# Kernel optimization log

Measured on AMD Instinct MI355X. Metric: run time of the kernel, lower is better.

The kernel has to match this reference:

```python
import jax, jax.numpy as jnp
import numpy as np

BETA = 0.9
TH = 1.0  # snn.Leaky default threshold
SPARSITY = 0.5


@jax.custom_vjp
def spike(x):
    # Heaviside spike; surrogate (atan, alpha=2) gradient as in snntorch default
    return (x > 0).astype(x.dtype)

def _spike_fwd(x):
    return spike(x), x

def _spike_bwd(x, g):
    return (g / (1.0 + (jnp.pi * x) ** 2),)

spike.defvjp(_spike_fwd, _spike_bwd)


def setup_inputs() -> dict:
    key = jax.random.key(0)
    ks = jax.random.split(key, 6)
    T, B, NIN, NH, NOUT = 50, 512, 784, 1000, 10

    def mk_w(k, o, i):
        k1, k2 = jax.random.split(k)
        w = jax.random.normal(k1, (o, i), jnp.float32) * (1.0 / np.sqrt(i))
        mask = (jax.random.uniform(k2, (o, i)) > SPARSITY).astype(jnp.float32)
        return w * mask

    x = jax.random.normal(ks[0], (T, B, NIN), jnp.float32)
    return dict(
        x=x,
        W0=mk_w(ks[1], NH, NIN), b0=jnp.zeros((NH,), jnp.float32),
        W1=mk_w(ks[2], NH, NH), b1=jnp.zeros((NH,), jnp.float32),
        W2=mk_w(ks[3], NH, NH), b2=jnp.zeros((NH,), jnp.float32),
        W3=mk_w(ks[4], NOUT, NH), b3=jnp.zeros((NOUT,), jnp.float32),
    )


def reference(x, W0, b0, W1, b1, W2, b2, W3, b3):
    params = ((W0, b0), (W1, b1), (W2, b2), (W3, b3))
    B = x.shape[1]
    mems0 = tuple(jnp.zeros((B, W.shape[0]), x.dtype) for W, _ in params)

    def step(mems, xt):
        inp = xt
        new_mems, spks = [], []
        for (W, b), m in zip(params, mems):
            cur = inp @ W.T + b
            # snntorch Leaky (reset_mechanism='subtract'):
            # reset from previous mem (detached), then mem = beta*mem + I - reset*th
            reset = jax.lax.stop_gradient((m > TH).astype(x.dtype))
            m_new = BETA * m + cur - reset * TH
            s = spike(m_new - TH)
            new_mems.append(m_new)
            spks.append(s)
            inp = s
        return tuple(new_mems), (tuple(spks), tuple(new_mems))

    _, (spk_rec, mem_rec) = jax.lax.scan(step, mems0, x)
    # spk_rec/mem_rec: tuples of [T, B, dim] arrays per layer
    return (*spk_rec, *mem_rec)
```

## Files before the change

kernel.cpp:

```cpp
#include <hip/hip_runtime.h>


typedef int int4v  __attribute__((ext_vector_type(4)));
typedef int int16v __attribute__((ext_vector_type(16)));

#define XSCALE 68719476736.0
#define WSCALE 1099511627776.0
#define MT 25600

__global__ void wsplit_i8(const float* __restrict__ W, signed char* __restrict__ out,
                          int Nreal, int Npad, int K, int Kpad)
{
    int idx = blockIdx.x * blockDim.x + threadIdx.x;
    int total = Npad * Kpad;
    if (idx >= total) return;
    int n = idx / Kpad, k = idx - n * Kpad;
    long long v = 0;
    if (n < Nreal && k < K) v = __double2ll_rn((double)W[(size_t)n * K + k] * WSCALE);
    size_t plane = (size_t)total;
#pragma unroll
    for (int p = 0; p < 4; ++p) {
        int d = (int)(v & 255); if (d > 127) d -= 256;
        out[p * plane + idx] = (signed char)d;
        v = (v - d) >> 8;
    }
    out[4 * plane + idx] = (signed char)v;
}

__global__ void xsplit_all(const float* __restrict__ x, signed char* __restrict__ out)
{
    int idx = blockIdx.x * blockDim.x + threadIdx.x;
    if (idx >= MT * 832) return;
    int row = idx / 832, k = idx - row * 832;
    long long v = 0;
    if (k < 784) v = __double2ll_rn((double)x[(size_t)row * 784 + k] * XSCALE);
    const size_t plane = (size_t)MT * 832;
    signed char* o = out + idx;
#pragma unroll
    for (int p = 0; p < 4; ++p) {
        int d = (int)(v & 255); if (d > 127) d -= 256;
        o[p * plane] = (signed char)d;
        v = (v - d) >> 8;
    }
    o[4 * plane] = (signed char)v;
}

template<int NA, int KP, int CS>
__global__ __launch_bounds__(256)
void gemm32(const signed char* __restrict__ Ap, size_t planeA,
            const signed char* __restrict__ Wp, size_t planeW,
            double* __restrict__ curout)
{
    __shared__ __align__(16) signed char Wld[5 * 64 * 80];
    __shared__ __align__(16) signed char Ald[NA * 64 * 80];
    constexpr int NIT = KP / 64;

    const int tid = threadIdx.x;
    const int l   = tid & 63;
    const int w   = tid >> 6;
    const int wm  = (w & 1) * 32;
    const int wn  = (w >> 1) * 32;
    const int r32 = l & 31;
    const int h   = l >> 5;

    const int bm = blockIdx.y * 64;
    const int bn = blockIdx.x * 64;

    const int srow = tid >> 2;
    const int sc   = (tid & 3) * 16;

    const signed char* ag = Ap + (size_t)(bm + srow) * KP + sc;
    const signed char* wg = Wp + (size_t)(bn + srow) * KP + sc;

    int4v Ar[NA], Wr[5];
#pragma unroll
    for (int p = 0; p < 5; ++p)  Wr[p] = *(const int4v*)(wg + p * planeW);
#pragma unroll
    for (int p = 0; p < NA; ++p) Ar[p] = *(const int4v*)(ag + p * planeA);

    int16v acc[5];
#pragma unroll
    for (int s = 0; s < 5; ++s)
#pragma unroll
        for (int r = 0; r < 16; ++r) acc[s][r] = 0;

    for (int it = 0; it < NIT; ++it) {
        __syncthreads();
#pragma unroll
        for (int p = 0; p < 5; ++p)
            *(int4v*)&Wld[(p * 64 + srow) * 80 + sc] = Wr[p];
#pragma unroll
        for (int p = 0; p < NA; ++p)
            *(int4v*)&Ald[(p * 64 + srow) * 80 + sc] = Ar[p];
        __syncthreads();

        if (it + 1 < NIT) {
            int kb = (it + 1) * 64;
#pragma unroll
            for (int p = 0; p < 5; ++p)
                Wr[p] = *(const int4v*)(wg + kb + p * planeW);
#pragma unroll
            for (int p = 0; p < NA; ++p)
                Ar[p] = *(const int4v*)(ag + kb + p * planeA);
        }

#pragma unroll
        for (int k2 = 0; k2 < 2; ++k2) {
            const int off = k2 * 32 + 16 * h;
            if constexpr (NA == 5) {
                int4v af[5], bq[5];
#pragma unroll
                for (int p = 0; p < 5; ++p)
                    af[p] = *(const int4v*)&Ald[(p * 64 + wm + r32) * 80 + off];
#pragma unroll
                for (int q = 0; q < 5; ++q)
                    bq[q] = *(const int4v*)&Wld[(q * 64 + wn + r32) * 80 + off];
#pragma unroll
                for (int q = 0; q < 5; ++q)
#pragma unroll
                    for (int p = 0; p < 5; ++p)
                        if (p + q >= 4)
                            acc[p + q - 4] = __builtin_amdgcn_mfma_i32_32x32x32_i8(
                                af[p], bq[q], acc[p + q - 4], 0, 0, 0);
            } else {
                int4v a0 = *(const int4v*)&Ald[(wm + r32) * 80 + off];
#pragma unroll
                for (int q = 0; q < 5; ++q) {
                    int4v bq = *(const int4v*)&Wld[(q * 64 + wn + r32) * 80 + off];
                    acc[q] = __builtin_amdgcn_mfma_i32_32x32x32_i8(a0, bq, acc[q], 0, 0, 0);
                }
            }
        }
    }

    const int col = bn + wn + r32;
    if (col < CS) {
#pragma unroll
        for (int reg = 0; reg < 16; ++reg) {
            int row = bm + wm + (reg & 3) + 8 * (reg >> 2) + 4 * h;
            double v = (double)acc[4][reg];
            v = v * 256.0 + (double)acc[3][reg];
            v = v * 256.0 + (double)acc[2][reg];
            v = v * 256.0 + (double)acc[1][reg];
            v = v * 256.0 + (double)acc[0][reg];
            curout[(size_t)row * CS + col] = v * (NA == 5 ? 0x1p-44 : 0x1p-40);
        }
    }
}

template<int KP>
__global__ __launch_bounds__(256)
void gemm32w(const signed char* __restrict__ Asp,
             const signed char* __restrict__ Wp, size_t planeW,
             double* __restrict__ curout)
{
    __shared__ __align__(16) signed char Wld[2][5 * 64 * 80];
    __shared__ __align__(16) signed char Ald[2][128 * 80];
    constexpr int NIT = KP / 64;

    const int tid = threadIdx.x;
    const int l   = tid & 63;
    const int w   = tid >> 6;
    const int wm  = (w & 1) * 64;
    const int wn  = (w >> 1) * 32;
    const int r32 = l & 31;
    const int h   = l >> 5;

    const int bm = blockIdx.y * 128;
    const int bn = blockIdx.x * 64;

    const int srA = tid >> 1;
    const int scA = (tid & 1) * 32;
    const int srW = tid >> 2;
    const int scW = (tid & 3) * 16;

    const signed char* ag = Asp + (size_t)(bm + srA) * KP + scA;
    const signed char* wg = Wp  + (size_t)(bn + srW) * KP + scW;

    int4v Ar0 = *(const int4v*)(ag);
    int4v Ar1 = *(const int4v*)(ag + 16);
    int4v Wr[5];
#pragma unroll
    for (int p = 0; p < 5; ++p) Wr[p] = *(const int4v*)(wg + p * planeW);
#pragma unroll
    for (int p = 0; p < 5; ++p)
        *(int4v*)&Wld[0][(p * 64 + srW) * 80 + scW] = Wr[p];
    *(int4v*)&Ald[0][srA * 80 + scA]      = Ar0;
    *(int4v*)&Ald[0][srA * 80 + scA + 16] = Ar1;
    if (NIT > 1) {
        Ar0 = *(const int4v*)(ag + 64);
        Ar1 = *(const int4v*)(ag + 64 + 16);
#pragma unroll
        for (int p = 0; p < 5; ++p)
            Wr[p] = *(const int4v*)(wg + 64 + p * planeW);
    }
    __syncthreads();

    int16v acc[2][5];
#pragma unroll
    for (int mi = 0; mi < 2; ++mi)
#pragma unroll
        for (int s = 0; s < 5; ++s)
#pragma unroll
            for (int r = 0; r < 16; ++r) acc[mi][s][r] = 0;

    for (int it = 0; it < NIT; ++it) {
        const int cur = it & 1;

#pragma unroll
        for (int k2 = 0; k2 < 2; ++k2) {
            const int off = k2 * 32 + 16 * h;
            int4v bq[5];
#pragma unroll
            for (int q = 0; q < 5; ++q)
                bq[q] = *(const int4v*)&Wld[cur][(q * 64 + wn + r32) * 80 + off];
#pragma unroll
            for (int mi = 0; mi < 2; ++mi) {
                int4v a0 = *(const int4v*)&Ald[cur][(wm + mi * 32 + r32) * 80 + off];
#pragma unroll
                for (int q = 0; q < 5; ++q)
                    acc[mi][q] = __builtin_amdgcn_mfma_i32_32x32x32_i8(
                        a0, bq[q], acc[mi][q], 0, 0, 0);
            }
        }

        if (it + 1 < NIT) {
            const int nxt = cur ^ 1;
#pragma unroll
            for (int p = 0; p < 5; ++p)
                *(int4v*)&Wld[nxt][(p * 64 + srW) * 80 + scW] = Wr[p];
            *(int4v*)&Ald[nxt][srA * 80 + scA]      = Ar0;
            *(int4v*)&Ald[nxt][srA * 80 + scA + 16] = Ar1;
            if (it + 2 < NIT) {
                int kb = (it + 2) * 64;
                Ar0 = *(const int4v*)(ag + kb);
                Ar1 = *(const int4v*)(ag + kb + 16);
#pragma unroll
                for (int p = 0; p < 5; ++p)
                    Wr[p] = *(const int4v*)(wg + kb + p * planeW);
            }
            __syncthreads();
        }
    }

    const int col = bn + wn + r32;
#pragma unroll
    for (int mi = 0; mi < 2; ++mi)
#pragma unroll
        for (int reg = 0; reg < 16; ++reg) {
            int row = bm + wm + mi * 32 + (reg & 3) + 8 * (reg >> 2) + 4 * h;
            double v = (double)acc[mi][4][reg];
            v = v * 256.0 + (double)acc[mi][3][reg];
            v = v * 256.0 + (double)acc[mi][2][reg];
            v = v * 256.0 + (double)acc[mi][1][reg];
            v = v * 256.0 + (double)acc[mi][0][reg];
            curout[(size_t)row * 1024 + col] = v * 0x1p-40;
        }
}

__global__ __launch_bounds__(256)
void if_update(const double* __restrict__ cur, const float* __restrict__ bias,
               float* __restrict__ spk, float* __restrict__ mem,
               signed char* __restrict__ spk_i8)
{
    int idx = blockIdx.x * blockDim.x + threadIdx.x;
    if (idx >= 512 * 512) return;
    int row = idx >> 9, col = (idx & 511) * 2;
    if (col >= 1000) {
        for (int t = 0; t < 50; ++t)
            *(short*)&spk_i8[((size_t)t * 512 + row) * 1024 + col] = 0;
        return;
    }
    double mp0 = 0.0, mp1 = 0.0;
    double bs0 = (double)bias[col], bs1 = (double)bias[col + 1];
    for (int t = 0; t < 50; ++t) {
        double2 c = *(const double2*)&cur[((size_t)t * 512 + row) * 1024 + col];
        double rst0 = (mp0 > 1.0) ? 1.0 : 0.0;
        double rst1 = (mp1 > 1.0) ? 1.0 : 0.0;
        double mn0 = 0.9 * mp0 + (c.x + bs0) - rst0;
        double mn1 = 0.9 * mp1 + (c.y + bs1) - rst1;
        int s0 = (mn0 > 1.0) ? 1 : 0;
        int s1 = (mn1 > 1.0) ? 1 : 0;
        size_t o = ((size_t)t * 512 + row) * 1000 + col;
        *(float2*)&spk[o] = make_float2((float)s0, (float)s1);
        *(float2*)&mem[o] = make_float2((float)mn0, (float)mn1);
        *(short*)&spk_i8[((size_t)t * 512 + row) * 1024 + col] =
            (short)(s0 | (s1 << 8));
        mp0 = mn0; mp1 = mn1;
    }
}

__global__ __launch_bounds__(256)
void if3_kernel(const double* __restrict__ cur3, const float* __restrict__ bias,
                float* __restrict__ spk3, float* __restrict__ mem3)
{
    int idx = blockIdx.x * blockDim.x + threadIdx.x;
    if (idx >= 5120) return;
    int brow = idx / 10, col = idx - brow * 10;
    double bs = (double)bias[col];
    double mp = 0.0;
    for (int t = 0; t < 50; ++t) {
        double c   = cur3[((size_t)t * 512 + brow) * 16 + col] + bs;
        double rst = (mp > 1.0) ? 1.0 : 0.0;
        double mn  = 0.9 * mp + c - rst;
        size_t o   = (size_t)t * 5120 + (size_t)brow * 10 + col;
        spk3[o] = (mn > 1.0) ? 1.0f : 0.0f;
        mem3[o] = (float)mn;
        mp = mn;
    }
}

extern "C" void kernel_launch(void* const* d_in, const int* in_sizes, int n_in,
                              void* d_out, int out_size, void* d_ws, size_t ws_size,
                              hipStream_t stream)
{
    const float* x  = (const float*)d_in[0];
    const float* W0 = (const float*)d_in[1];
    const float* b0 = (const float*)d_in[2];
    const float* W1 = (const float*)d_in[3];
    const float* b1 = (const float*)d_in[4];
    const float* W2 = (const float*)d_in[5];
    const float* b2 = (const float*)d_in[6];
    const float* W3 = (const float*)d_in[7];
    const float* b3 = (const float*)d_in[8];
    float* out = (float*)d_out;

    const int T = 50;
    const size_t LNH = (size_t)512 * 1000;
    const size_t LNO = (size_t)512 * 10;

    float* spk0 = out;
    float* spk1 = spk0 + (size_t)T * LNH;
    float* spk2 = spk1 + (size_t)T * LNH;
    float* spk3 = spk2 + (size_t)T * LNH;
    float* mem0 = spk3 + (size_t)T * LNO;
    float* mem1 = mem0 + (size_t)T * LNH;
    float* mem2 = mem1 + (size_t)T * LNH;
    float* mem3 = mem2 + (size_t)T * LNH;

    double* cur = (double*)d_ws;
    signed char* W0d = (signed char*)(cur + (size_t)MT * 1024);
    signed char* W1d = W0d + (size_t)5 * 1024 * 832;
    signed char* W2d = W1d + (size_t)5 * 1024 * 1024;
    signed char* W3d = W2d + (size_t)5 * 1024 * 1024;
    signed char* xsb = W3d + (size_t)5 * 64 * 1024;
    signed char* sp0 = xsb + (size_t)5 * MT * 832;
    signed char* sp1 = sp0 + (size_t)MT * 1024;
    signed char* sp2 = sp1 + (size_t)MT * 1024;

    wsplit_i8<<<(1024 * 832  + 255) / 256, 256, 0, stream>>>(W0, W0d, 1000, 1024, 784,  832);
    wsplit_i8<<<(1024 * 1024 + 255) / 256, 256, 0, stream>>>(W1, W1d, 1000, 1024, 1000, 1024);
    wsplit_i8<<<(1024 * 1024 + 255) / 256, 256, 0, stream>>>(W2, W2d, 1000, 1024, 1000, 1024);
    wsplit_i8<<<(64 * 1024   + 255) / 256, 256, 0, stream>>>(W3, W3d, 10,   64,   1000, 1024);

    xsplit_all<<<(MT * 832 + 255) / 256, 256, 0, stream>>>(x, xsb);

    const size_t plA0 = (size_t)MT * 832;
    const size_t plW0 = (size_t)1024 * 832;
    const size_t plWH = (size_t)1024 * 1024;
    const size_t plW3 = (size_t)64 * 1024;

    dim3 blk(256);
    dim3 g0(16, MT / 64);
    dim3 gW(16, MT / 128);
    dim3 g3(1, MT / 64);

    gemm32<5, 832, 1024><<<g0, blk, 0, stream>>>(xsb, plA0, W0d, plW0, cur);
    if_update<<<1024, 256, 0, stream>>>(cur, b0, spk0, mem0, sp0);
    gemm32w<1024><<<gW, blk, 0, stream>>>(sp0, W1d, plWH, cur);
    if_update<<<1024, 256, 0, stream>>>(cur, b1, spk1, mem1, sp1);
    gemm32w<1024><<<gW, blk, 0, stream>>>(sp1, W2d, plWH, cur);
    if_update<<<1024, 256, 0, stream>>>(cur, b2, spk2, mem2, sp2);
    gemm32<1, 1024, 16><<<g3, blk, 0, stream>>>(sp2, 0, W3d, plW3, cur);
    if3_kernel<<<20, 256, 0, stream>>>(cur, b3, spk3, mem3);
}
```

Measured before the change: 1.061 ms.

## Pre-tile hidden-layer operands and stream them into LDS with direct global loads

```diff
diff --git a/kernel.cpp b/kernel.cpp
--- a/kernel.cpp
+++ b/kernel.cpp
@@ -7,6 +7,13 @@
 #define XSCALE 68719476736.0
 #define WSCALE 1099511627776.0
 #define MT 25600
+
+__device__ __forceinline__ void gload16(const signed char* g, signed char* l)
+{
+    __builtin_amdgcn_global_load_lds(
+        (const __attribute__((address_space(1))) void*)g,
+        (__attribute__((address_space(3))) void*)l, 16, 0, 0);
+}
 
 __global__ void wsplit_i8(const float* __restrict__ W, signed char* __restrict__ out,
                           int Nreal, int Npad, int K, int Kpad)
@@ -25,6 +32,34 @@
         v = (v - d) >> 8;
     }
     out[4 * plane + idx] = (signed char)v;
+}
+
+__global__ void wsplit_tw(const float* __restrict__ W, signed char* __restrict__ out)
+{
+    int idx = blockIdx.x * blockDim.x + threadIdx.x;
+    if (idx >= 65536) return;
+    int q4 = idx & 3, row = (idx >> 2) & 63, kb = (idx >> 8) & 15, nt = idx >> 12;
+    int n = nt * 64 + row;
+    long long v[16];
+#pragma unroll
+    for (int j = 0; j < 16; ++j) {
+        int k = kb * 64 + q4 * 16 + j;
+        float wv = (n < 1000 && k < 1000) ? W[(size_t)n * 1000 + k] : 0.f;
+        v[j] = __double2ll_rn((double)wv * WSCALE);
+    }
+    signed char* tile = out + (size_t)(nt * 16 + kb) * 25600;
+#pragma unroll
+    for (int p = 0; p < 5; ++p) {
+        signed char pk[16];
+#pragma unroll
+        for (int j = 0; j < 16; ++j) {
+            int d;
+            if (p < 4) { d = (int)(v[j] & 255); if (d > 127) d -= 256; v[j] = (v[j] - d) >> 8; }
+            else d = (int)v[j];
+            pk[j] = (signed char)d;
+        }
+        *(int4v*)&tile[(p * 64 + row) * 80 + q4 * 16] = *(const int4v*)pk;
+    }
 }
 
 __global__ void xsplit_all(const float* __restrict__ x, signed char* __restrict__ out)
@@ -148,15 +183,14 @@
     }
 }
 
-template<int KP>
 __global__ __launch_bounds__(256)
-void gemm32w(const signed char* __restrict__ Asp,
-             const signed char* __restrict__ Wp, size_t planeW,
-             double* __restrict__ curout)
-{
-    __shared__ __align__(16) signed char Wld[2][5 * 64 * 80];
-    __shared__ __align__(16) signed char Ald[2][128 * 80];
-    constexpr int NIT = KP / 64;
+void gemm32wa(const signed char* __restrict__ At,
+              const signed char* __restrict__ Wt,
+              double* __restrict__ curout)
+{
+    constexpr int NIT = 16;
+    __shared__ __align__(16) signed char B0[36864];
+    __shared__ __align__(16) signed char B1[36864];
 
     const int tid = threadIdx.x;
     const int l   = tid & 63;
@@ -166,35 +200,24 @@
     const int r32 = l & 31;
     const int h   = l >> 5;
 
-    const int bm = blockIdx.y * 128;
-    const int bn = blockIdx.x * 64;
-
-    const int srA = tid >> 1;
-    const int scA = (tid & 1) * 32;
-    const int srW = tid >> 2;
-    const int scW = (tid & 3) * 16;
-
-    const signed char* ag = Asp + (size_t)(bm + srA) * KP + scA;
-    const signed char* wg = Wp  + (size_t)(bn + srW) * KP + scW;
-
-    int4v Ar0 = *(const int4v*)(ag);
-    int4v Ar1 = *(const int4v*)(ag + 16);
-    int4v Wr[5];
-#pragma unroll
-    for (int p = 0; p < 5; ++p) Wr[p] = *(const int4v*)(wg + p * planeW);
-#pragma unroll
-    for (int p = 0; p < 5; ++p)
-        *(int4v*)&Wld[0][(p * 64 + srW) * 80 + scW] = Wr[p];
-    *(int4v*)&Ald[0][srA * 80 + scA]      = Ar0;
-    *(int4v*)&Ald[0][srA * 80 + scA + 16] = Ar1;
-    if (NIT > 1) {
-        Ar0 = *(const int4v*)(ag + 64);
-        Ar1 = *(const int4v*)(ag + 64 + 16);
-#pragma unroll
-        for (int p = 0; p < 5; ++p)
-            Wr[p] = *(const int4v*)(wg + 64 + p * planeW);
-    }
-    __syncthreads();
+    const int nt = blockIdx.x, mt = blockIdx.y;
+    const signed char* wtile = Wt + (size_t)nt * (16 * 25600);
+    const signed char* atile = At + (size_t)mt * (16 * 10240);
+
+    auto issue = [&](int kb, signed char* buf) {
+        const signed char* wsrc = wtile + kb * 25600;
+        const signed char* asrc = atile + kb * 10240;
+#pragma unroll
+        for (int j = 0; j < 9; ++j) {
+            int c = w + 4 * j;
+            const signed char* g;
+            signed char* d;
+            if (c < 25) { g = wsrc + c * 1024;                     d = buf + c * 1024; }
+            else        { int ac = c - 25;
+                          g = asrc + (ac < 10 ? ac : 9) * 1024;    d = buf + 25600 + ac * 1024; }
+            gload16(g + l * 16, d);
+        }
+    };
 
     int16v acc[2][5];
 #pragma unroll
@@ -204,51 +227,47 @@
 #pragma unroll
             for (int r = 0; r < 16; ++r) acc[mi][s][r] = 0;
 
+    issue(0, B0);
+    issue(1, B1);
+    asm volatile("s_waitcnt vmcnt(9)" ::: "memory");
+    __builtin_amdgcn_s_barrier();
+
     for (int it = 0; it < NIT; ++it) {
-        const int cur = it & 1;
-
+        signed char* buf = (it & 1) ? B1 : B0;
 #pragma unroll
         for (int k2 = 0; k2 < 2; ++k2) {
             const int off = k2 * 32 + 16 * h;
             int4v bq[5];
 #pragma unroll
             for (int q = 0; q < 5; ++q)
-                bq[q] = *(const int4v*)&Wld[cur][(q * 64 + wn + r32) * 80 + off];
+                bq[q] = *(const int4v*)&buf[(q * 64 + wn + r32) * 80 + off];
 #pragma unroll
             for (int mi = 0; mi < 2; ++mi) {
-                int4v a0 = *(const int4v*)&Ald[cur][(wm + mi * 32 + r32) * 80 + off];
+                int4v a0 = *(const int4v*)&buf[25600 + (wm + mi * 32 + r32) * 80 + off];
 #pragma unroll
                 for (int q = 0; q < 5; ++q)
                     acc[mi][q] = __builtin_amdgcn_mfma_i32_32x32x32_i8(
                         a0, bq[q], acc[mi][q], 0, 0, 0);
             }
         }
-
         if (it + 1 < NIT) {
-            const int nxt = cur ^ 1;
-#pragma unroll
-            for (int p = 0; p < 5; ++p)
-                *(int4v*)&Wld[nxt][(p * 64 + srW) * 80 + scW] = Wr[p];
-            *(int4v*)&Ald[nxt][srA * 80 + scA]      = Ar0;
-            *(int4v*)&Ald[nxt][srA * 80 + scA + 16] = Ar1;
+            __builtin_amdgcn_s_barrier();
             if (it + 2 < NIT) {
-                int kb = (it + 2) * 64;
-                Ar0 = *(const int4v*)(ag + kb);
-                Ar1 = *(const int4v*)(ag + kb + 16);
-#pragma unroll
-                for (int p = 0; p < 5; ++p)
-                    Wr[p] = *(const int4v*)(wg + kb + p * planeW);
+                issue(it + 2, buf);
+                asm volatile("s_waitcnt vmcnt(9)" ::: "memory");
+            } else {
+                asm volatile("s_waitcnt vmcnt(0)" ::: "memory");
             }
-            __syncthreads();
-        }
-    }
-
-    const int col = bn + wn + r32;
+            __builtin_amdgcn_s_barrier();
+        }
+    }
+
+    const int col = nt * 64 + wn + r32;
 #pragma unroll
     for (int mi = 0; mi < 2; ++mi)
 #pragma unroll
         for (int reg = 0; reg < 16; ++reg) {
-            int row = bm + wm + mi * 32 + (reg & 3) + 8 * (reg >> 2) + 4 * h;
+            int row = mt * 128 + wm + mi * 32 + (reg & 3) + 8 * (reg >> 2) + 4 * h;
             double v = (double)acc[mi][4][reg];
             v = v * 256.0 + (double)acc[mi][3][reg];
             v = v * 256.0 + (double)acc[mi][2][reg];
@@ -258,6 +277,7 @@
         }
 }
 
+template<bool TILED>
 __global__ __launch_bounds__(256)
 void if_update(const double* __restrict__ cur, const float* __restrict__ bias,
                float* __restrict__ spk, float* __restrict__ mem,
@@ -266,9 +286,19 @@
     int idx = blockIdx.x * blockDim.x + threadIdx.x;
     if (idx >= 512 * 512) return;
     int row = idx >> 9, col = (idx & 511) * 2;
+
+    auto sp_off = [&](int t, int c) -> size_t {
+        if constexpr (TILED) {
+            int trow = t * 512 + row;
+            return ((size_t)((trow >> 7) * 16 + (c >> 6)) * 128 + (trow & 127)) * 80 + (c & 63);
+        } else {
+            return ((size_t)t * 512 + row) * 1024 + c;
+        }
+    };
+
     if (col >= 1000) {
         for (int t = 0; t < 50; ++t)
-            *(short*)&spk_i8[((size_t)t * 512 + row) * 1024 + col] = 0;
+            *(short*)&spk_i8[sp_off(t, col)] = 0;
         return;
     }
     double mp0 = 0.0, mp1 = 0.0;
@@ -284,8 +314,7 @@
         size_t o = ((size_t)t * 512 + row) * 1000 + col;
         *(float2*)&spk[o] = make_float2((float)s0, (float)s1);
         *(float2*)&mem[o] = make_float2((float)mn0, (float)mn1);
-        *(short*)&spk_i8[((size_t)t * 512 + row) * 1024 + col] =
-            (short)(s0 | (s1 << 8));
+        *(short*)&spk_i8[sp_off(t, col)] = (short)(s0 | (s1 << 8));
         mp0 = mn0; mp1 = mn1;
     }
 }
@@ -340,24 +369,23 @@
 
     double* cur = (double*)d_ws;
     signed char* W0d = (signed char*)(cur + (size_t)MT * 1024);
-    signed char* W1d = W0d + (size_t)5 * 1024 * 832;
-    signed char* W2d = W1d + (size_t)5 * 1024 * 1024;
-    signed char* W3d = W2d + (size_t)5 * 1024 * 1024;
+    signed char* W1t = W0d + (size_t)5 * 1024 * 832;
+    signed char* W2t = W1t + (size_t)16 * 16 * 25600;
+    signed char* W3d = W2t + (size_t)16 * 16 * 25600;
     signed char* xsb = W3d + (size_t)5 * 64 * 1024;
     signed char* sp0 = xsb + (size_t)5 * MT * 832;
-    signed char* sp1 = sp0 + (size_t)MT * 1024;
-    signed char* sp2 = sp1 + (size_t)MT * 1024;
-
-    wsplit_i8<<<(1024 * 832  + 255) / 256, 256, 0, stream>>>(W0, W0d, 1000, 1024, 784,  832);
-    wsplit_i8<<<(1024 * 1024 + 255) / 256, 256, 0, stream>>>(W1, W1d, 1000, 1024, 1000, 1024);
-    wsplit_i8<<<(1024 * 1024 + 255) / 256, 256, 0, stream>>>(W2, W2d, 1000, 1024, 1000, 1024);
-    wsplit_i8<<<(64 * 1024   + 255) / 256, 256, 0, stream>>>(W3, W3d, 10,   64,   1000, 1024);
+    signed char* sp1 = sp0 + (size_t)200 * 16 * 10240;
+    signed char* sp2 = sp1 + (size_t)200 * 16 * 10240;
+
+    wsplit_i8<<<(1024 * 832 + 255) / 256, 256, 0, stream>>>(W0, W0d, 1000, 1024, 784, 832);
+    wsplit_tw<<<65536 / 256, 256, 0, stream>>>(W1, W1t);
+    wsplit_tw<<<65536 / 256, 256, 0, stream>>>(W2, W2t);
+    wsplit_i8<<<(64 * 1024 + 255) / 256, 256, 0, stream>>>(W3, W3d, 10, 64, 1000, 1024);
 
     xsplit_all<<<(MT * 832 + 255) / 256, 256, 0, stream>>>(x, xsb);
 
     const size_t plA0 = (size_t)MT * 832;
     const size_t plW0 = (size_t)1024 * 832;
-    const size_t plWH = (size_t)1024 * 1024;
     const size_t plW3 = (size_t)64 * 1024;
 
     dim3 blk(256);
@@ -366,11 +394,11 @@
     dim3 g3(1, MT / 64);
 
     gemm32<5, 832, 1024><<<g0, blk, 0, stream>>>(xsb, plA0, W0d, plW0, cur);
-    if_update<<<1024, 256, 0, stream>>>(cur, b0, spk0, mem0, sp0);
-    gemm32w<1024><<<gW, blk, 0, stream>>>(sp0, W1d, plWH, cur);
-    if_update<<<1024, 256, 0, stream>>>(cur, b1, spk1, mem1, sp1);
-    gemm32w<1024><<<gW, blk, 0, stream>>>(sp1, W2d, plWH, cur);
-    if_update<<<1024, 256, 0, stream>>>(cur, b2, spk2, mem2, sp2);
+    if_update<true><<<1024, 256, 0, stream>>>(cur, b0, spk0, mem0, sp0);
+    gemm32wa<<<gW, blk, 0, stream>>>(sp0, W1t, cur);
+    if_update<true><<<1024, 256, 0, stream>>>(cur, b1, spk1, mem1, sp1);
+    gemm32wa<<<gW, blk, 0, stream>>>(sp1, W2t, cur);
+    if_update<false><<<1024, 256, 0, stream>>>(cur, b2, spk2, mem2, sp2);
     gemm32<1, 1024, 16><<<g3, blk, 0, stream>>>(sp2, 0, W3d, plW3, cur);
     if3_kernel<<<20, 256, 0, stream>>>(cur, b3, spk3, mem3);
 }
```

Result: slower. 1.296 ms (+22.1%).
